# Kernel tuning notes

Measured on AMD Instinct MI355X. Metric: run time of the kernel, lower is better.

Reference implementation:

```python
import jax, jax.numpy as jnp
import numpy as np

EPS = 1e-15
PROJ_EPS = 4e-3  # float32 boundary eps (geoopt convention)

def _artanh(x):
    return jnp.arctanh(jnp.clip(x, -1.0 + 1e-7, 1.0 - 1e-7))

def _norm(x, axis=-1):
    return jnp.maximum(jnp.sqrt(jnp.sum(x * x, axis=axis, keepdims=True)), EPS)

def expmap0(u, c):
    sc = jnp.sqrt(c)
    n = _norm(u)
    return jnp.tanh(sc * n) * u / (sc * n)

def project(x, c):
    n = _norm(x)
    maxn = (1.0 - PROJ_EPS) / jnp.sqrt(c)
    return jnp.where(n > maxn, x / n * maxn, x)

def mobius_pointwise_mul(w, x, c):
    sc = jnp.sqrt(c)
    wx = w * x
    xn = _norm(x)
    wxn = _norm(wx)
    return jnp.tanh(wxn / xn * _artanh(sc * xn)) * wx / (wxn * sc)

def mobius_add(x, y, c):
    x2 = jnp.sum(x * x, -1, keepdims=True)
    y2 = jnp.sum(y * y, -1, keepdims=True)
    xy = jnp.sum(x * y, -1, keepdims=True)
    num = (1.0 + 2.0 * c * xy + c * y2) * x + (1.0 - c * x2) * y
    den = 1.0 + 2.0 * c * xy + (c ** 2) * x2 * y2
    return num / jnp.maximum(den, EPS)

def logmap0(y, c):
    sc = jnp.sqrt(c)
    n = _norm(y)
    return _artanh(sc * n) * y / (sc * n)

def weighted_midpoint_batched(mix, c):
    # mix: (B, D, L); feature axis = 1 (torch call: dim=0 per sample), reduce over L.
    lam = 2.0 / jnp.maximum(1.0 - c * jnp.sum(mix * mix, axis=1, keepdims=True), EPS)  # (B,1,L)
    nom = jnp.sum(lam * mix, axis=2)          # (B, D)
    den = jnp.sum(lam - 1.0, axis=2)          # (B, 1)
    den = jnp.where(den >= 0, jnp.maximum(den, 1e-10), jnp.minimum(den, -1e-10))
    tm = nom / den                            # (B, D) "two_mean"
    # mobius_scalar_mul(0.5, tm)
    sc = jnp.sqrt(c)
    n = _norm(tm)
    return jnp.tanh(0.5 * _artanh(sc * n)) * tm / (sc * n)

def setup_inputs() -> dict:
    key = jax.random.key(0)
    ks = jax.random.split(key, 7)
    B, O, L, D = 64, 1, 1024, 1024
    return {
        "query": jax.random.normal(ks[0], (B, O, D), jnp.float32),
        "context": jax.random.normal(ks[1], (B, L, D), jnp.float32),
        "delta_t": jax.random.uniform(ks[2], (B, 1, L), jnp.float32),
        "c": jnp.ones((1,), jnp.float32),
        "W_in": jax.random.normal(ks[3], (D, D), jnp.float32) / np.float32(np.sqrt(D)),
        "W_out": jax.random.normal(ks[4], (D, 2 * D), jnp.float32) / np.float32(np.sqrt(2 * D)),
        "ae": jax.random.normal(ks[5], (B, 1, 1), jnp.float32) * 0.1,
        "ab": jax.random.normal(ks[6], (B, 1, 1), jnp.float32) * 0.1,
    }

def reference(query, context, delta_t, c, W_in, W_out, ae, ab):
    # linear_in (attention_type='general'): no bias
    q = jnp.einsum('bod,ed->boe', query, W_in)                     # (B,O,D)
    scores = jnp.einsum('bod,bld->bol', q, context)                # (B,O,L)
    aw = jax.nn.softmax(scores, axis=-1)
    aw = project(expmap0(aw, c), c)                                # hyperbolic attn weights
    ctx_t = jnp.transpose(context, (0, 2, 1))                      # (B,D,L)
    mix = project(mobius_pointwise_mul(aw, ctx_t, c), c)           # (B,D,L)
    bt = jnp.exp(-ab * delta_t)                                    # (B,1,L)
    bt = project(expmap0(bt, c), c)
    tmp = project(mobius_pointwise_mul(ae, mix, c), c)
    tmp = project(mobius_pointwise_mul(tmp, bt, c), c)
    term2 = jax.nn.relu(tmp)
    mix = project(mobius_add(mix, term2, c), c)
    fin = weighted_midpoint_batched(mix, c)[:, None, :]            # (B,1,D)
    mixl = logmap0(fin, c)
    combined = jnp.concatenate([mixl, q], axis=-1)                 # (B,1,2D)
    out = jnp.tanh(jnp.einsum('boe,de->bod', combined, W_out))     # (B,1,D)
    return (out, aw)
```

## Files before the change

### kernel.cpp

```cpp
#include <hip/hip_runtime.h>
#include <math.h>

#define BB 64
#define LL 1024
#define DD 1024

typedef __attribute__((ext_vector_type(4))) _Float16 half4;
typedef __attribute__((ext_vector_type(8))) _Float16 half8;
typedef __attribute__((ext_vector_type(4))) float f32x4;

__device__ __forceinline__ float artanh_c(float x){
  x = fminf(fmaxf(x, -1.f + 1e-7f), 1.f - 1e-7f);
  return 0.5f * __logf((1.f + x) / (1.f - x));
}

__device__ __forceinline__ float wave_sum(float v){
  #pragma unroll
  for(int o = 32; o > 0; o >>= 1) v += __shfl_down(v, o, 64);
  return v;
}

__device__ __forceinline__ float block_sum4(float v, float* red){
  v = wave_sum(v);
  int wid = threadIdx.x >> 6, lane = threadIdx.x & 63;
  if(lane == 0) red[wid] = v;
  __syncthreads();
  float t = red[0] + red[1] + red[2] + red[3];
  __syncthreads();
  return t;
}

__device__ __forceinline__ float block_max4(float v, float* red){
  #pragma unroll
  for(int o = 32; o > 0; o >>= 1) v = fmaxf(v, __shfl_down(v, o, 64));
  int wid = threadIdx.x >> 6, lane = threadIdx.x & 63;
  if(lane == 0) red[wid] = v;
  __syncthreads();
  float t = fmaxf(fmaxf(red[0], red[1]), fmaxf(red[2], red[3]));
  __syncthreads();
  return t;
}

__global__ void k_qproj(const float* __restrict__ query, const float* __restrict__ Win,
                        float* __restrict__ q){
  int wave = threadIdx.x >> 6, lane = threadIdx.x & 63;
  int e = blockIdx.x * 4 + wave;
  int b0 = blockIdx.y * 16;
  const float4* Wr = (const float4*)(Win + (size_t)e * DD);
  float4 w[4];
  #pragma unroll
  for(int j = 0; j < 4; j++) w[j] = Wr[j * 64 + lane];
  for(int bb = 0; bb < 16; bb++){
    int b = b0 + bb;
    const float4* qr = (const float4*)(query + (size_t)b * DD);
    float acc = 0.f;
    #pragma unroll
    for(int j = 0; j < 4; j++){
      float4 v = qr[j * 64 + lane];
      acc += w[j].x * v.x + w[j].y * v.y + w[j].z * v.z + w[j].w * v.w;
    }
    acc = wave_sum(acc);
    if(lane == 0) q[b * DD + e] = acc;
  }
}

__global__ void k_scores(const float* __restrict__ qv, const float* __restrict__ ctx,
                         float* __restrict__ scores, _Float16* __restrict__ ctx16){
  int b = blockIdx.y;
  int wave = threadIdx.x >> 6, lane = threadIdx.x & 63;
  int l = blockIdx.x * 4 + wave;
  __shared__ float4 qs4[DD / 4];
  qs4[threadIdx.x] = ((const float4*)(qv + (size_t)b * DD))[threadIdx.x];
  __syncthreads();
  const f32x4* cr = (const f32x4*)(ctx + ((size_t)b * LL + l) * DD);
  half4* c16 = (half4*)(ctx16 + ((size_t)b * LL + l) * DD);
  float acc = 0.f;
  #pragma unroll
  for(int it = 0; it < 4; it++){
    int idx = it * 64 + lane;
    f32x4 v = __builtin_nontemporal_load(&cr[idx]);
    float4 qq = qs4[idx];
    acc += qq.x * v.x + qq.y * v.y + qq.z * v.z + qq.w * v.w;
    half4 h;
    h.x = (_Float16)v.x; h.y = (_Float16)v.y; h.z = (_Float16)v.z; h.w = (_Float16)v.w;
    c16[idx] = h;
  }
  acc = wave_sum(acc);
  if(lane == 0) scores[b * LL + l] = acc;
}

__global__ void k_softmax_tr(const float* __restrict__ scores, const float* __restrict__ dt,
                             const float* __restrict__ ab, const float* __restrict__ cp,
                             float* __restrict__ awt, float* __restrict__ aw_out,
                             float* __restrict__ btt, float* __restrict__ btn){
  __shared__ float red[4];
  int b = blockIdx.x, tid = threadIdx.x;
  float c = cp[0], sc = sqrtf(c), maxn = (1.f - 4e-3f) / sc;
  float4 s = ((const float4*)(scores + (size_t)b * LL))[tid];
  float m = block_max4(fmaxf(fmaxf(s.x, s.y), fmaxf(s.z, s.w)), red);
  float4 e;
  e.x = __expf(s.x - m); e.y = __expf(s.y - m); e.z = __expf(s.z - m); e.w = __expf(s.w - m);
  float Z = block_sum4(e.x + e.y + e.z + e.w, red);
  float inv = 1.f / Z;
  float4 aw;
  aw.x = e.x * inv; aw.y = e.y * inv; aw.z = e.z * inv; aw.w = e.w * inv;
  float S = block_sum4(aw.x * aw.x + aw.y * aw.y + aw.z * aw.z + aw.w * aw.w, red);
  float n = fmaxf(sqrtf(S), 1e-15f);
  float tau = tanhf(sc * n) / (sc * n);
  float n1 = fmaxf(tau * sqrtf(S), 1e-15f);
  float s1 = n1 > maxn ? maxn / n1 : 1.f;
  float f = tau * s1;
  float4 awf;
  awf.x = f * aw.x; awf.y = f * aw.y; awf.z = f * aw.z; awf.w = f * aw.w;
  ((float4*)(awt + (size_t)b * LL))[tid] = awf;
  ((float4*)(aw_out + (size_t)b * LL))[tid] = awf;
  float4 d4 = ((const float4*)(dt + (size_t)b * LL))[tid];
  float abv = ab[b];
  float4 bv;
  bv.x = __expf(-abv * d4.x); bv.y = __expf(-abv * d4.y);
  bv.z = __expf(-abv * d4.z); bv.w = __expf(-abv * d4.w);
  float S2 = block_sum4(bv.x * bv.x + bv.y * bv.y + bv.z * bv.z + bv.w * bv.w, red);
  float n2 = fmaxf(sqrtf(S2), 1e-15f);
  float tau2 = tanhf(sc * n2) / (sc * n2);
  float nb = fmaxf(tau2 * sqrtf(S2), 1e-15f);
  float s2f = nb > maxn ? maxn / nb : 1.f;
  float f2 = tau2 * s2f;
  float4 btf;
  btf.x = f2 * bv.x; btf.y = f2 * bv.y; btf.z = f2 * bv.z; btf.w = f2 * bv.w;
  ((float4*)(btt + (size_t)b * LL))[tid] = btf;
  if(tid == 0) btn[b] = fmaxf(f2 * sqrtf(S2), 1e-15f);
}

__global__ __launch_bounds__(256) void k_stats(const _Float16* __restrict__ ctx16,
                        const float* __restrict__ awt,
                        const float* __restrict__ btt, float* __restrict__ stats16){
  int tid = threadIdx.x;
  int b = blockIdx.x;
  int oct = tid & 127, h = tid >> 7;
  int l0 = blockIdx.y * 128;
  __shared__ float w2_[128], w2b_[128], w2b2_[128];
  if(tid < 128){
    float w = awt[b * LL + l0 + tid], bt = btt[b * LL + l0 + tid];
    float w2 = w * w;
    w2_[tid] = w2; w2b_[tid] = w2 * bt; w2b2_[tid] = w2 * bt * bt;
  }
  __syncthreads();
  const half8* cpx = (const half8*)(ctx16 + ((size_t)b * LL + l0 + h * 64) * DD) + oct;
  float r2[8] = {0,0,0,0,0,0,0,0}, p2[8] = {0,0,0,0,0,0,0,0};
  float s3p[8] = {0,0,0,0,0,0,0,0}, s3m[8] = {0,0,0,0,0,0,0,0};
  float s5p[8] = {0,0,0,0,0,0,0,0}, s5m[8] = {0,0,0,0,0,0,0,0};
  #pragma unroll 8
  for(int i = 0; i < 64; i++){
    half8 hv = cpx[(size_t)i * 128];
    int li = h * 64 + i;
    float w2 = w2_[li], w2b = w2b_[li], w2b2 = w2b2_[li];
    #pragma unroll
    for(int j = 0; j < 8; j++){
      float r = (float)hv[j];
      float rsq = r * r;
      float rp2 = r > 0.f ? rsq : 0.f;
      float rn2 = rsq - rp2;
      r2[j] += rsq;
      p2[j] = fmaf(w2, rsq, p2[j]);
      s3p[j] = fmaf(w2b2, rp2, s3p[j]);
      s3m[j] = fmaf(w2b2, rn2, s3m[j]);
      s5p[j] = fmaf(w2b, rp2, s5p[j]);
      s5m[j] = fmaf(w2b, rn2, s5m[j]);
    }
  }
  float* sl = stats16 + (((size_t)b * 16 + (size_t)blockIdx.y * 2 + h) * 6) * DD + oct * 8;
  #define ST_(sidx, arr) { float4* o = (float4*)(sl + (sidx) * DD); \
    o[0] = make_float4(arr[0], arr[1], arr[2], arr[3]); \
    o[1] = make_float4(arr[4], arr[5], arr[6], arr[7]); }
  ST_(0, r2) ST_(1, p2) ST_(2, s3p) ST_(3, s3m) ST_(4, s5p) ST_(5, s5m)
  #undef ST_
}

__global__ void k_finish(const float* __restrict__ stats16, const float* __restrict__ ae,
                         const float* __restrict__ btn, const float* __restrict__ cp,
                         float* __restrict__ rowsc){
  int row = blockIdx.x * 256 + threadIdx.x;
  int b = row >> 10;
  int d = row & (DD - 1);
  float c = cp[0], sc = sqrtf(c), maxn = (1.f - 4e-3f) / sc;
  const float* st = stats16 + (size_t)b * 16 * 6 * DD + d;
  float r2 = 0.f, p2 = 0.f, s3p = 0.f, s3m = 0.f, s5p = 0.f, s5m = 0.f;
  #pragma unroll
  for(int g = 0; g < 16; g++){
    const float* sg = st + (size_t)g * 6 * DD;
    r2 += sg[0]; p2 += sg[DD]; s3p += sg[2 * DD];
    s3m += sg[3 * DD]; s5p += sg[4 * DD]; s5m += sg[5 * DD];
  }
  float sp2 = sqrtf(p2);
  float xn  = fmaxf(sqrtf(r2), 1e-15f);
  float wxn = fmaxf(sp2, 1e-15f);
  float at1 = artanh_c(sc * xn);
  float alpha = tanhf(wxn / xn * at1) / (wxn * sc);
  float n1 = fmaxf(alpha * sp2, 1e-15f);
  float beta = alpha * (n1 > maxn ? maxn / n1 : 1.f);
  float aeb = ae[b];
  float mixn_raw = beta * sp2;
  float xn2  = fmaxf(mixn_raw, 1e-15f);
  float wxn2 = fmaxf(fabsf(aeb) * mixn_raw, 1e-15f);
  float at2 = artanh_c(sc * xn2);
  float coef_t = tanhf(wxn2 / xn2 * at2) * aeb * beta / (wxn2 * sc);
  float n2 = fmaxf(fabsf(coef_t) * sp2, 1e-15f);
  float g = coef_t * (n2 > maxn ? maxn / n2 : 1.f);
  float s3 = s3p + s3m;
  float sq3 = sqrtf(s3);
  float xn3 = btn[b];
  float wxn3 = fmaxf(fabsf(g) * sq3, 1e-15f);
  float at3 = artanh_c(sc * xn3);
  float coef2 = tanhf(wxn3 / xn3 * at3) * g / (wxn3 * sc);
  float n3 = fmaxf(fabsf(coef2) * sq3, 1e-15f);
  float k = coef2 * (n3 > maxn ? maxn / n3 : 1.f);
  bool kp = k > 0.f;
  float ssel  = kp ? s3p : s3m;
  float s5sel = kp ? s5p : s5m;
  float y2 = k * k * ssel;
  float xy = beta * k * s5sel;
  float x2 = beta * beta * p2;
  float A  = 1.f + 2.f * c * xy + c * y2;
  float Bc = 1.f - c * x2;
  float den = 1.f + 2.f * c * xy + c * c * x2 * y2;
  den = fmaxf(den, 1e-15f);
  float U0 = A * beta / den;
  float V0 = Bc * k / den;
  float nf2 = U0 * U0 * p2 + 2.f * U0 * V0 * s5sel + V0 * V0 * ssel;
  float nf = fmaxf(sqrtf(nf2), 1e-15f);
  float s4 = nf > maxn ? maxn / nf : 1.f;
  float U = U0 * s4, V = V0 * s4;
  float4* out4 = (float4*)(rowsc + (size_t)row * 4);
  *out4 = make_float4(U, kp ? V : 0.f, kp ? 0.f : V, 0.f);
}

__global__ __launch_bounds__(256) void k_mixagg(const _Float16* __restrict__ ctx16,
                         const float* __restrict__ awt, const float* __restrict__ btt,
                         const float* __restrict__ rowsc, const float* __restrict__ cp,
                         float* __restrict__ lam_out, float* __restrict__ nom32){
  __shared__ float aw_s[32], bt_s[32], lam_s[32];
  int b = blockIdx.y;
  int l0 = blockIdx.x * 32;
  int tid = threadIdx.x, wave = tid >> 6, lane = tid & 63;
  float c = cp[0];
  if(tid < 32){ aw_s[tid] = awt[b * LL + l0 + tid]; bt_s[tid] = btt[b * LL + l0 + tid]; }
  float U1[2][8], Vp1[2][8], Vm1[2][8];
  const float4* rp = (const float4*)rowsc + (size_t)b * DD;
  #pragma unroll
  for(int it = 0; it < 2; it++){
    int o = it * 64 + lane;
    #pragma unroll
    for(int j = 0; j < 8; j++){
      float4 t = rp[o * 8 + j];
      U1[it][j] = t.x; Vp1[it][j] = t.y; Vm1[it][j] = t.z;
    }
  }
  float U2[4], Vp2[4], Vm2[4];
  #pragma unroll
  for(int j = 0; j < 4; j++){
    float4 t = rp[tid * 4 + j];
    U2[j] = t.x; Vp2[j] = t.y; Vm2[j] = t.z;
  }
  __syncthreads();
  const half8* cb8 = (const half8*)(ctx16 + (size_t)b * LL * DD);
  #pragma unroll
  for(int rr = 0; rr < 8; rr++){
    int r = wave + rr * 4;
    int l = l0 + r;
    float w = aw_s[r], bt = bt_s[r];
    float acc = 0.f;
    #pragma unroll
    for(int it = 0; it < 2; it++){
      half8 hv = cb8[(size_t)l * 128 + it * 64 + lane];
      #pragma unroll
      for(int j = 0; j < 8; j++){
        float rc = (float)hv[j];
        float t = rc > 0.f ? Vp1[it][j] : Vm1[it][j];
        float uv = fmaf(bt, t, U1[it][j]);
        float mvs = rc * uv;
        acc = fmaf(mvs, mvs, acc);
      }
    }
    acc = wave_sum(acc);
    if(lane == 0){
      float lv = 2.f / fmaxf(1.f - c * (w * w) * acc, 1e-15f);
      lam_s[r] = lv;
      lam_out[b * LL + l] = lv;
    }
  }
  __syncthreads();
  float acc2[4] = {0, 0, 0, 0};
  const half4* cb4 = (const half4*)(ctx16 + (size_t)b * LL * DD);
  #pragma unroll 4
  for(int r = 0; r < 32; r++){
    float bt = bt_s[r];
    float lw = lam_s[r] * aw_s[r];
    half4 hv = cb4[(size_t)(l0 + r) * 256 + tid];
    float rx[4] = {(float)hv.x, (float)hv.y, (float)hv.z, (float)hv.w};
    #pragma unroll
    for(int j = 0; j < 4; j++){
      float rc = rx[j];
      float t = rc > 0.f ? Vp2[j] : Vm2[j];
      float mv = rc * fmaf(bt, t, U2[j]);
      acc2[j] = fmaf(lw, mv, acc2[j]);
    }
  }
  ((float4*)(nom32 + ((size_t)b * 32 + blockIdx.x) * DD))[tid] =
      make_float4(acc2[0], acc2[1], acc2[2], acc2[3]);
}

__global__ void k_mid(const float* __restrict__ nom32, const float* __restrict__ lam,
                      const float* __restrict__ qv, const float* __restrict__ cp,
                      float* __restrict__ comb){
  __shared__ float red[4];
  int b = blockIdx.x, tid = threadIdx.x;
  float c = cp[0], sc = sqrtf(c);
  float4 lv = ((const float4*)(lam + (size_t)b * LL))[tid];
  float dsum = block_sum4(lv.x + lv.y + lv.z + lv.w - 4.f, red);
  float den = dsum >= 0.f ? fmaxf(dsum, 1e-10f) : fminf(dsum, -1e-10f);
  float nx = 0.f, ny = 0.f, nz = 0.f, nw = 0.f;
  #pragma unroll
  for(int k = 0; k < 32; k++){
    float4 t = ((const float4*)(nom32 + ((size_t)b * 32 + k) * DD))[tid];
    nx += t.x; ny += t.y; nz += t.z; nw += t.w;
  }
  float tx = nx / den, ty = ny / den, tz = nz / den, tw = nw / den;
  float S = block_sum4(tx * tx + ty * ty + tz * tz + tw * tw, red);
  float n = fmaxf(sqrtf(S), 1e-15f);
  float at = artanh_c(sc * n);
  float mu = tanhf(0.5f * at) / (sc * n);
  float n2 = fmaxf(mu * sqrtf(S), 1e-15f);
  float nu = artanh_c(sc * n2) / (sc * n2);
  float f = nu * mu;
  float4 q4 = ((const float4*)(qv + (size_t)b * DD))[tid];
  ((float4*)(comb + (size_t)b * 2 * DD))[tid] = make_float4(f * tx, f * ty, f * tz, f * tw);
  ((float4*)(comb + (size_t)b * 2 * DD + DD))[tid] = q4;
}

__global__ void k_out(const float* __restrict__ comb, const float* __restrict__ Wout,
                      float* __restrict__ outp){
  int wave = threadIdx.x >> 6, lane = threadIdx.x & 63;
  int d = blockIdx.x * 4 + wave;
  int b0 = blockIdx.y * 16;
  const float4* Wr = (const float4*)(Wout + (size_t)d * 2 * DD);
  float4 w[8];
  #pragma unroll
  for(int j = 0; j < 8; j++) w[j] = Wr[j * 64 + lane];
  for(int bb = 0; bb < 16; bb++){
    int b = b0 + bb;
    const float4* cb = (const float4*)(comb + (size_t)b * 2 * DD);
    float acc = 0.f;
    #pragma unroll
    for(int j = 0; j < 8; j++){
      float4 v = cb[j * 64 + lane];
      acc += w[j].x * v.x + w[j].y * v.y + w[j].z * v.z + w[j].w * v.w;
    }
    acc = wave_sum(acc);
    if(lane == 0) outp[b * DD + d] = tanhf(acc);
  }
}

extern "C" void kernel_launch(void* const* d_in, const int* in_sizes, int n_in,
                              void* d_out, int out_size, void* d_ws, size_t ws_size,
                              hipStream_t stream) {
  const float* query = (const float*)d_in[0];
  const float* ctx   = (const float*)d_in[1];
  const float* dt    = (const float*)d_in[2];
  const float* cp    = (const float*)d_in[3];
  const float* Win   = (const float*)d_in[4];
  const float* Wout  = (const float*)d_in[5];
  const float* ae    = (const float*)d_in[6];
  const float* ab    = (const float*)d_in[7];
  float* out = (float*)d_out;
  float* ws  = (float*)d_ws;

  float* q_       = ws;
  float* awt_     = ws + 65536;
  float* btt_     = ws + 131072;
  float* btn_     = ws + 196608;
  float* scores_  = ws + 196736;
  float* rowsc_   = ws + 262272;
  float* comb_    = ws + 524416;
  float* stats16_ = ws + 655488;
  float* nom32_   = ws + 6946944;
  _Float16* ctx16_ = (_Float16*)(ws + 9044096);
  float* lam_ = scores_;

  k_qproj     <<<dim3(256, 4),  256, 0, stream>>>(query, Win, q_);
  k_scores    <<<dim3(256, BB), 256, 0, stream>>>(q_, ctx, scores_, ctx16_);
  k_softmax_tr<<<BB,            256, 0, stream>>>(scores_, dt, ab, cp, awt_, out + BB * DD, btt_, btn_);
  k_stats     <<<dim3(BB, 8),   256, 0, stream>>>(ctx16_, awt_, btt_, stats16_);
  k_finish    <<<256,           256, 0, stream>>>(stats16_, ae, btn_, cp, rowsc_);
  k_mixagg    <<<dim3(32, BB),  256, 0, stream>>>(ctx16_, awt_, btt_, rowsc_, cp, lam_, nom32_);
  k_mid       <<<BB,            256, 0, stream>>>(nom32_, lam_, q_, cp, comb_);
  k_out       <<<dim3(256, 4),  256, 0, stream>>>(comb_, Wout, out);
}
```

Measured before the change: 498.3 us.

## Rebalance work: more rows per scores block, finer stats split, paired row loads in mixagg

k_scores now has each wave process 8 context rows instead of 1, cutting the grid from 256x64 to 32x64 blocks and amortising the per-block query staging. k_stats splits L into 16 chunks of 64 rows instead of 8 chunks of 128, doubling the block count for more parallelism. In exchange, k_finish must reduce twice as many partial-stat slices and the workspace layout is shifted. k_mixagg's first pass handles two rows per iteration with all four loads issued up front, to raise memory-level parallelism.

```diff
diff --git a/kernel.cpp b/kernel.cpp
--- a/kernel.cpp
+++ b/kernel.cpp
@@ -64,29 +64,34 @@
   }
 }
 
-__global__ void k_scores(const float* __restrict__ qv, const float* __restrict__ ctx,
+__global__ __launch_bounds__(256) void k_scores(const float* __restrict__ qv,
+                         const float* __restrict__ ctx,
                          float* __restrict__ scores, _Float16* __restrict__ ctx16){
   int b = blockIdx.y;
-  int wave = threadIdx.x >> 6, lane = threadIdx.x & 63;
-  int l = blockIdx.x * 4 + wave;
+  int tid = threadIdx.x, wave = tid >> 6, lane = tid & 63;
+  int l0 = blockIdx.x * 32 + wave * 8;
   __shared__ float4 qs4[DD / 4];
-  qs4[threadIdx.x] = ((const float4*)(qv + (size_t)b * DD))[threadIdx.x];
-  __syncthreads();
-  const f32x4* cr = (const f32x4*)(ctx + ((size_t)b * LL + l) * DD);
-  half4* c16 = (half4*)(ctx16 + ((size_t)b * LL + l) * DD);
-  float acc = 0.f;
-  #pragma unroll
-  for(int it = 0; it < 4; it++){
-    int idx = it * 64 + lane;
-    f32x4 v = __builtin_nontemporal_load(&cr[idx]);
-    float4 qq = qs4[idx];
-    acc += qq.x * v.x + qq.y * v.y + qq.z * v.z + qq.w * v.w;
-    half4 h;
-    h.x = (_Float16)v.x; h.y = (_Float16)v.y; h.z = (_Float16)v.z; h.w = (_Float16)v.w;
-    c16[idx] = h;
-  }
-  acc = wave_sum(acc);
-  if(lane == 0) scores[b * LL + l] = acc;
+  qs4[tid] = ((const float4*)(qv + (size_t)b * DD))[tid];
+  __syncthreads();
+  #pragma unroll 2
+  for(int rr = 0; rr < 8; rr++){
+    int l = l0 + rr;
+    const f32x4* cr = (const f32x4*)(ctx + ((size_t)b * LL + l) * DD);
+    half4* c16 = (half4*)(ctx16 + ((size_t)b * LL + l) * DD);
+    float acc = 0.f;
+    #pragma unroll
+    for(int it = 0; it < 4; it++){
+      int idx = it * 64 + lane;
+      f32x4 v = __builtin_nontemporal_load(&cr[idx]);
+      float4 qq = qs4[idx];
+      acc += qq.x * v.x + qq.y * v.y + qq.z * v.z + qq.w * v.w;
+      half4 h;
+      h.x = (_Float16)v.x; h.y = (_Float16)v.y; h.z = (_Float16)v.z; h.w = (_Float16)v.w;
+      c16[idx] = h;
+    }
+    acc = wave_sum(acc);
+    if(lane == 0) scores[b * LL + l] = acc;
+  }
 }
 
 __global__ void k_softmax_tr(const float* __restrict__ scores, const float* __restrict__ dt,
@@ -133,26 +138,26 @@
 
 __global__ __launch_bounds__(256) void k_stats(const _Float16* __restrict__ ctx16,
                         const float* __restrict__ awt,
-                        const float* __restrict__ btt, float* __restrict__ stats16){
+                        const float* __restrict__ btt, float* __restrict__ stats32){
   int tid = threadIdx.x;
   int b = blockIdx.x;
   int oct = tid & 127, h = tid >> 7;
-  int l0 = blockIdx.y * 128;
-  __shared__ float w2_[128], w2b_[128], w2b2_[128];
-  if(tid < 128){
+  int l0 = blockIdx.y * 64;
+  __shared__ float w2_[64], w2b_[64], w2b2_[64];
+  if(tid < 64){
     float w = awt[b * LL + l0 + tid], bt = btt[b * LL + l0 + tid];
     float w2 = w * w;
     w2_[tid] = w2; w2b_[tid] = w2 * bt; w2b2_[tid] = w2 * bt * bt;
   }
   __syncthreads();
-  const half8* cpx = (const half8*)(ctx16 + ((size_t)b * LL + l0 + h * 64) * DD) + oct;
+  const half8* cpx = (const half8*)(ctx16 + ((size_t)b * LL + l0 + h * 32) * DD) + oct;
   float r2[8] = {0,0,0,0,0,0,0,0}, p2[8] = {0,0,0,0,0,0,0,0};
   float s3p[8] = {0,0,0,0,0,0,0,0}, s3m[8] = {0,0,0,0,0,0,0,0};
   float s5p[8] = {0,0,0,0,0,0,0,0}, s5m[8] = {0,0,0,0,0,0,0,0};
   #pragma unroll 8
-  for(int i = 0; i < 64; i++){
+  for(int i = 0; i < 32; i++){
     half8 hv = cpx[(size_t)i * 128];
-    int li = h * 64 + i;
+    int li = h * 32 + i;
     float w2 = w2_[li], w2b = w2b_[li], w2b2 = w2b2_[li];
     #pragma unroll
     for(int j = 0; j < 8; j++){
@@ -168,7 +173,7 @@
       s5m[j] = fmaf(w2b, rn2, s5m[j]);
     }
   }
-  float* sl = stats16 + (((size_t)b * 16 + (size_t)blockIdx.y * 2 + h) * 6) * DD + oct * 8;
+  float* sl = stats32 + (((size_t)b * 32 + (size_t)blockIdx.y * 2 + h) * 6) * DD + oct * 8;
   #define ST_(sidx, arr) { float4* o = (float4*)(sl + (sidx) * DD); \
     o[0] = make_float4(arr[0], arr[1], arr[2], arr[3]); \
     o[1] = make_float4(arr[4], arr[5], arr[6], arr[7]); }
@@ -176,17 +181,17 @@
   #undef ST_
 }
 
-__global__ void k_finish(const float* __restrict__ stats16, const float* __restrict__ ae,
+__global__ void k_finish(const float* __restrict__ stats32, const float* __restrict__ ae,
                          const float* __restrict__ btn, const float* __restrict__ cp,
                          float* __restrict__ rowsc){
   int row = blockIdx.x * 256 + threadIdx.x;
   int b = row >> 10;
   int d = row & (DD - 1);
   float c = cp[0], sc = sqrtf(c), maxn = (1.f - 4e-3f) / sc;
-  const float* st = stats16 + (size_t)b * 16 * 6 * DD + d;
+  const float* st = stats32 + (size_t)b * 32 * 6 * DD + d;
   float r2 = 0.f, p2 = 0.f, s3p = 0.f, s3m = 0.f, s5p = 0.f, s5m = 0.f;
-  #pragma unroll
-  for(int g = 0; g < 16; g++){
+  #pragma unroll 4
+  for(int g = 0; g < 32; g++){
     const float* sg = st + (size_t)g * 6 * DD;
     r2 += sg[0]; p2 += sg[DD]; s3p += sg[2 * DD];
     s3m += sg[3 * DD]; s5p += sg[4 * DD]; s5m += sg[5 * DD];
@@ -264,28 +269,46 @@
   __syncthreads();
   const half8* cb8 = (const half8*)(ctx16 + (size_t)b * LL * DD);
   #pragma unroll
-  for(int rr = 0; rr < 8; rr++){
-    int r = wave + rr * 4;
-    int l = l0 + r;
-    float w = aw_s[r], bt = bt_s[r];
-    float acc = 0.f;
-    #pragma unroll
-    for(int it = 0; it < 2; it++){
-      half8 hv = cb8[(size_t)l * 128 + it * 64 + lane];
-      #pragma unroll
-      for(int j = 0; j < 8; j++){
-        float rc = (float)hv[j];
-        float t = rc > 0.f ? Vp1[it][j] : Vm1[it][j];
-        float uv = fmaf(bt, t, U1[it][j]);
-        float mvs = rc * uv;
-        acc = fmaf(mvs, mvs, acc);
-      }
-    }
-    acc = wave_sum(acc);
+  for(int rr = 0; rr < 4; rr++){
+    int rA = wave + rr * 8, rB = rA + 4;
+    int lA = l0 + rA, lB = l0 + rB;
+    half8 a0 = cb8[(size_t)lA * 128 + lane];
+    half8 a1 = cb8[(size_t)lA * 128 + 64 + lane];
+    half8 b0 = cb8[(size_t)lB * 128 + lane];
+    half8 b1 = cb8[(size_t)lB * 128 + 64 + lane];
+    float accA = 0.f, accB = 0.f;
+    #pragma unroll
+    for(int j = 0; j < 8; j++){
+      float ra0 = (float)a0[j];
+      float t0 = ra0 > 0.f ? Vp1[0][j] : Vm1[0][j];
+      float uvA0 = fmaf(bt_s[rA], t0, U1[0][j]);
+      float mA0 = ra0 * uvA0;
+      accA = fmaf(mA0, mA0, accA);
+      float ra1 = (float)a1[j];
+      float t1 = ra1 > 0.f ? Vp1[1][j] : Vm1[1][j];
+      float uvA1 = fmaf(bt_s[rA], t1, U1[1][j]);
+      float mA1 = ra1 * uvA1;
+      accA = fmaf(mA1, mA1, accA);
+      float rb0 = (float)b0[j];
+      float t2 = rb0 > 0.f ? Vp1[0][j] : Vm1[0][j];
+      float uvB0 = fmaf(bt_s[rB], t2, U1[0][j]);
+      float mB0 = rb0 * uvB0;
+      accB = fmaf(mB0, mB0, accB);
+      float rb1 = (float)b1[j];
+      float t3 = rb1 > 0.f ? Vp1[1][j] : Vm1[1][j];
+      float uvB1 = fmaf(bt_s[rB], t3, U1[1][j]);
+      float mB1 = rb1 * uvB1;
+      accB = fmaf(mB1, mB1, accB);
+    }
+    accA = wave_sum(accA);
+    accB = wave_sum(accB);
     if(lane == 0){
-      float lv = 2.f / fmaxf(1.f - c * (w * w) * acc, 1e-15f);
-      lam_s[r] = lv;
-      lam_out[b * LL + l] = lv;
+      float wA = aw_s[rA], wB = aw_s[rB];
+      float lvA = 2.f / fmaxf(1.f - c * (wA * wA) * accA, 1e-15f);
+      float lvB = 2.f / fmaxf(1.f - c * (wB * wB) * accB, 1e-15f);
+      lam_s[rA] = lvA; lam_s[rB] = lvB;
+      lam_out[b * LL + lA] = lvA;
+      lam_out[b * LL + lB] = lvB;
     }
   }
   __syncthreads();
@@ -381,16 +404,16 @@
   float* scores_  = ws + 196736;
   float* rowsc_   = ws + 262272;
   float* comb_    = ws + 524416;
-  float* stats16_ = ws + 655488;
-  float* nom32_   = ws + 6946944;
-  _Float16* ctx16_ = (_Float16*)(ws + 9044096);
+  float* stats32_ = ws + 655488;
+  float* nom32_   = ws + 13238400;
+  _Float16* ctx16_ = (_Float16*)(ws + 15335552);
   float* lam_ = scores_;
 
   k_qproj     <<<dim3(256, 4),  256, 0, stream>>>(query, Win, q_);
-  k_scores    <<<dim3(256, BB), 256, 0, stream>>>(q_, ctx, scores_, ctx16_);
+  k_scores    <<<dim3(32, BB),  256, 0, stream>>>(q_, ctx, scores_, ctx16_);
   k_softmax_tr<<<BB,            256, 0, stream>>>(scores_, dt, ab, cp, awt_, out + BB * DD, btt_, btn_);
-  k_stats     <<<dim3(BB, 8),   256, 0, stream>>>(ctx16_, awt_, btt_, stats16_);
-  k_finish    <<<256,           256, 0, stream>>>(stats16_, ae, btn_, cp, rowsc_);
+  k_stats     <<<dim3(BB, 16),  256, 0, stream>>>(ctx16_, awt_, btt_, stats32_);
+  k_finish    <<<256,           256, 0, stream>>>(stats32_, ae, btn_, cp, rowsc_);
   k_mixagg    <<<dim3(32, BB),  256, 0, stream>>>(ctx16_, awt_, btt_, rowsc_, cp, lam_, nom32_);
   k_mid       <<<BB,            256, 0, stream>>>(nom32_, lam_, q_, cp, comb_);
   k_out       <<<dim3(256, 4),  256, 0, stream>>>(comb_, Wout, out);
```

New measurement: 501.5 us. No clear change (+0.6%).
